# Kernel tuning notes

Hardware: AMD Instinct MI355X
Metric: run time of the kernel (lower is better)

## Reference

```python
import jax, jax.numpy as jnp
import numpy as np

N, F, M, E = 8192, 256, 128, 131072


def setup_inputs() -> dict:
    key = jax.random.key(0)
    k = jax.random.split(key, 6)
    x = jax.random.normal(k[0], (N, F), dtype=jnp.float32)
    edge_index = jax.random.randint(k[1], (2, E), 0, N, dtype=jnp.int64)
    eps = jax.random.normal(k[2], (N, M), dtype=jnp.float32)
    # small init scale so sigmoid(z_i . z_j) isn't saturated
    W_mu = jax.random.normal(k[3], (F, M), dtype=jnp.float32) * 0.05
    b_mu = jnp.zeros((M,), dtype=jnp.float32)
    W_sig = jax.random.normal(k[4], (F, M), dtype=jnp.float32) * 0.05
    b_sig = jnp.zeros((M,), dtype=jnp.float32)
    return {"x": x, "edge_index": edge_index, "eps": eps,
            "W_mu": W_mu, "b_mu": b_mu, "W_sig": W_sig, "b_sig": b_sig}


def reference(x, edge_index, eps, W_mu, b_mu, W_sig, b_sig):
    # Gaussian encoder: Normal(mu, exp(logstd)), Independent over latent dim
    mu = x @ W_mu + b_mu                      # [N, M]
    logstd = x @ W_sig + b_sig                # [N, M]
    sigma = jnp.exp(logstd)
    z = mu + sigma * eps                      # rsample, [N, M]

    # decoder.probability(dot(z_i, z_j)) = sigmoid(logit); vectorized as Z @ Z.T
    logits = z @ z.T                          # [N, N]

    # symmetric adjacency labels from edge_index (either direction counts)
    src, dst = edge_index[0], edge_index[1]
    adj = jnp.zeros((N, N), dtype=jnp.float32)
    adj = adj.at[src, dst].set(1.0)
    adj = adj.at[dst, src].set(1.0)

    # BCE(sigmoid(s), y) summed over unordered pairs i < j (stable logits form)
    per_pair = jax.nn.softplus(logits) - adj * logits  # = -[y log p + (1-y) log(1-p)]
    triu = jnp.triu(jnp.ones((N, N), dtype=bool), k=1)
    bce = jnp.sum(jnp.where(triu, per_pair, 0.0))

    # sum_i KL( N(mu_i, sigma_i) || N(0, I) )
    kl = jnp.sum(0.5 * (sigma * sigma + mu * mu - 1.0) - logstd)

    return bce + 0.001 * kl
```

## Files before the change

### kernel.cpp

```cpp
#include <hip/hip_runtime.h>

#define NN 8192
#define FF 256
#define MM 128
#define HSLOTS 262144

typedef __attribute__((ext_vector_type(8))) short bf16x8;
typedef __attribute__((ext_vector_type(4))) float f32x4;

#define P_KL    0
#define P_EDGE  (64 * 16)
#define P_SP    (128 * 16)
#define Z_OFF   16384
#define Z_BYTES (NN * MM * 2)
#define HASH_OFF (Z_OFF + Z_BYTES)
#define WT_OFF  (HASH_OFF + HSLOTS * 4)
#define WT_BYTES (MM * FF * 2)

__device__ __forceinline__ float wave_reduce(float v) {
    #pragma unroll
    for (int off = 32; off > 0; off >>= 1) v += __shfl_down(v, off);
    return v;
}
__device__ __forceinline__ unsigned short f2bf(float f) {
    unsigned int u = __float_as_uint(f);
    u += 0x7fffu + ((u >> 16) & 1u);
    return (unsigned short)(u >> 16);
}
__device__ __forceinline__ int4 pack8(float4 a, float4 b) {
    int4 p;
    p.x = (int)f2bf(a.x) | ((int)f2bf(a.y) << 16);
    p.y = (int)f2bf(a.z) | ((int)f2bf(a.w) << 16);
    p.z = (int)f2bf(b.x) | ((int)f2bf(b.y) << 16);
    p.w = (int)f2bf(b.z) | ((int)f2bf(b.w) << 16);
    return p;
}

__global__ __launch_bounds__(256)
void prep_w(const float* __restrict__ Wmu, const float* __restrict__ Wsg,
            unsigned short* __restrict__ WmuT, unsigned short* __restrict__ WsgT,
            float* __restrict__ part, unsigned int* __restrict__ ht) {
    const int t = blockIdx.x * 256 + threadIdx.x;
    const int n = t >> 8, f = t & 255;
    WmuT[t] = f2bf(Wmu[f * MM + n]);
    WsgT[t] = f2bf(Wsg[f * MM + n]);
    if (t < 4096) part[t] = 0.f;
    uint4 z4 = {0u, 0u, 0u, 0u};
    ((uint4*)ht)[t * 2]     = z4;
    ((uint4*)ht)[t * 2 + 1] = z4;
}

#define XP_I4 33
#define XP_S  264

__global__ __launch_bounds__(256)
void encoder_mfma(const float* __restrict__ x, const float* __restrict__ eps,
                  const unsigned short* __restrict__ WmuT,
                  const unsigned short* __restrict__ WsgT,
                  const float* __restrict__ bmu, const float* __restrict__ bsg,
                  unsigned short* __restrict__ zb, float* __restrict__ part) {
    __shared__ int4 ax[16 * XP_I4];
    __shared__ float red[4];
    const int tid = threadIdx.x;
    const int wid = tid >> 6, lane = tid & 63;
    const int l15 = lane & 15, quad = lane >> 4;
    const int row0 = blockIdx.x * 16;

    {
        const int r = tid >> 4, ch = tid & 15;
        const float4* g0 = (const float4*)(x + (size_t)(row0 + r) * FF + ch * 8);
        const float4* g1 = (const float4*)(x + (size_t)(row0 + r) * FF + (ch + 16) * 8);
        ax[r * XP_I4 + ch]      = pack8(g0[0], g0[1]);
        ax[r * XP_I4 + ch + 16] = pack8(g1[0], g1[1]);
    }
    __syncthreads();

    const short* sax = (const short*)ax;
    const int4* wtm = (const int4*)WmuT;
    const int4* wts = (const int4*)WsgT;

    f32x4 zero4 = {0.f, 0.f, 0.f, 0.f};
    f32x4 accm[2], accl[2];
    accm[0] = accm[1] = accl[0] = accl[1] = zero4;

    #pragma unroll
    for (int ks = 0; ks < 8; ++ks) {
        const bf16x8 a = *(const bf16x8*)&sax[l15 * XP_S + ks * 32 + quad * 8];
        #pragma unroll
        for (int j = 0; j < 2; ++j) {
            const int n = wid * 32 + j * 16 + l15;
            const bf16x8 bmf = *(const bf16x8*)&wtm[n * 32 + ks * 4 + quad];
            const bf16x8 bsf = *(const bf16x8*)&wts[n * 32 + ks * 4 + quad];
            accm[j] = __builtin_amdgcn_mfma_f32_16x16x32_bf16(a, bmf, accm[j], 0, 0, 0);
            accl[j] = __builtin_amdgcn_mfma_f32_16x16x32_bf16(a, bsf, accl[j], 0, 0, 0);
        }
    }

    float klp = 0.f;
    #pragma unroll
    for (int j = 0; j < 2; ++j) {
        const int col = wid * 32 + j * 16 + l15;
        const float bm = bmu[col], bs = bsg[col];
        #pragma unroll
        for (int r = 0; r < 4; ++r) {
            const int row = row0 + quad * 4 + r;
            const float mu = accm[j][r] + bm;
            const float ls = accl[j][r] + bs;
            const float sg = __expf(ls);
            const float zz = fmaf(sg, eps[(size_t)row * MM + col], mu);
            zb[(size_t)row * MM + col] = f2bf(zz);
            klp += 0.5f * (sg * sg + mu * mu - 1.f) - ls;
        }
    }

    klp = wave_reduce(klp);
    if (lane == 0) red[wid] = klp;
    __syncthreads();
    if (tid == 0)
        atomicAdd(&part[P_KL + (blockIdx.x & 63) * 16],
                  red[0] + red[1] + red[2] + red[3]);
}

__device__ __forceinline__ float dotpair(unsigned int a, unsigned int b) {
    const float al = __uint_as_float(a << 16);
    const float ah = __uint_as_float(a & 0xffff0000u);
    const float bl = __uint_as_float(b << 16);
    const float bh = __uint_as_float(b & 0xffff0000u);
    return fmaf(al, bl, ah * bh);
}

__global__ __launch_bounds__(256)
void edge_kernel(const int* __restrict__ ei, int E,
                 const unsigned short* __restrict__ zb,
                 unsigned int* __restrict__ ht, float* __restrict__ part) {
    const int e = blockIdx.x * 256 + threadIdx.x;
    float contrib = 0.f;
    if (e < E) {
        const int i = ei[e];
        const int j = ei[E + e];
        if (i != j) {
            const int a = min(i, j), b = max(i, j);
            const unsigned int key = (unsigned int)a * NN + b;
            unsigned int slot = (key * 2654435761u) & (HSLOTS - 1);
            bool first = false;
            for (;;) {
                const unsigned int old = atomicCAS(&ht[slot], 0u, key);
                if (old == 0u) { first = true; break; }
                if (old == key) break;
                slot = (slot + 1) & (HSLOTS - 1);
            }
            if (first) {
                const uint4* za = (const uint4*)(zb + (size_t)a * MM);
                const uint4* zc = (const uint4*)(zb + (size_t)b * MM);
                float s = 0.f;
                #pragma unroll
                for (int q = 0; q < MM / 8; ++q) {
                    const uint4 ua = za[q], ub = zc[q];
                    s += dotpair(ua.x, ub.x) + dotpair(ua.y, ub.y)
                       + dotpair(ua.z, ub.z) + dotpair(ua.w, ub.w);
                }
                contrib = s;
            }
        }
    }
    contrib = wave_reduce(contrib);
    if ((threadIdx.x & 63) == 0)
        atomicAdd(&part[P_EDGE + (blockIdx.x & 63) * 16], contrib);
}

__global__ __launch_bounds__(256, 3)
void tile_kernel(const unsigned short* __restrict__ zb, float* __restrict__ part) {
    const int bi = blockIdx.y, bj = blockIdx.x;
    if (bj < bi) return;

    __shared__ int4 la[128 * 8];
    __shared__ int4 lb[128 * 8];

    const int tid = threadIdx.x;
    const int wid = tid >> 6, lane = tid & 63;
    const int wm = wid >> 1, wn = wid & 1;
    const int l15 = lane & 15, quad = lane >> 4;
    const int xk = l15 & 7;

    const int4* ga = (const int4*)(zb + (size_t)bi * 128 * MM);
    const int4* gb = (const int4*)(zb + (size_t)bj * 128 * MM);

    f32x4 zero4 = {0.f, 0.f, 0.f, 0.f};
    f32x4 acc[4][4];
    #pragma unroll
    for (int i = 0; i < 4; ++i)
        #pragma unroll
        for (int j = 0; j < 4; ++j) acc[i][j] = zero4;

    const short* sa = (const short*)la;
    const short* sb = (const short*)lb;

    #pragma unroll
    for (int kc = 0; kc < 2; ++kc) {
        if (kc) __syncthreads();
        #pragma unroll
        for (int i = 0; i < 4; ++i) {
            const int c = tid + i * 256;
            const int row = c >> 3, ch = c & 7;
            const int sl = ch ^ (row & 7);
            la[row * 8 + sl] = ga[row * 16 + kc * 8 + ch];
            lb[row * 8 + sl] = gb[row * 16 + kc * 8 + ch];
        }
        __syncthreads();
        #pragma unroll
        for (int ks = 0; ks < 2; ++ks) {
            const int kq = ks * 4 + quad;
            bf16x8 af[4], bfr[4];
            #pragma unroll
            for (int t = 0; t < 4; ++t) {
                const int ar = wm * 64 + t * 16 + l15;
                af[t]  = *(const bf16x8*)&sa[ar * 64 + ((kq ^ xk) * 8)];
                const int br = wn * 64 + t * 16 + l15;
                bfr[t] = *(const bf16x8*)&sb[br * 64 + ((kq ^ xk) * 8)];
            }
            #pragma unroll
            for (int i = 0; i < 4; ++i)
                #pragma unroll
                for (int j = 0; j < 4; ++j)
                    acc[i][j] = __builtin_amdgcn_mfma_f32_16x16x32_bf16(
                        af[i], bfr[j], acc[i][j], 0, 0, 0);
        }
    }

    float tsum = 0.f;
    if (bi != bj) {
        #pragma unroll
        for (int i = 0; i < 4; ++i)
            #pragma unroll
            for (int j = 0; j < 4; ++j)
                #pragma unroll
                for (int r = 0; r < 4; ++r) {
                    const float v = acc[i][j][r];
                    const float e = __expf(-fabsf(v));
                    tsum += fmaxf(v, 0.f) + e * fmaf(e, -0.5f, 1.f);
                }
    } else {
        const int rbase = wm * 64 + quad * 4;
        const int cbase = wn * 64 + l15;
        #pragma unroll
        for (int i = 0; i < 4; ++i)
            #pragma unroll
            for (int j = 0; j < 4; ++j)
                #pragma unroll
                for (int r = 0; r < 4; ++r)
                    if (cbase + j * 16 > rbase + i * 16 + r) {
                        const float v = acc[i][j][r];
                        const float e = __expf(-fabsf(v));
                        tsum += fmaxf(v, 0.f) + e * fmaf(e, -0.5f, 1.f);
                    }
    }

    tsum = wave_reduce(tsum);
    if (lane == 0)
        atomicAdd(&part[P_SP + ((bi * 64 + bj + wid * 16) & 63) * 16], tsum);
}

__global__ void combine_kernel(const float* __restrict__ part,
                               float* __restrict__ out) {
    const int t = threadIdx.x;
    float v = part[P_SP + t * 16] - part[P_EDGE + t * 16]
            + 0.001f * part[P_KL + t * 16];
    v = wave_reduce(v);
    if (t == 0) out[0] = v;
}

extern "C" void kernel_launch(void* const* d_in, const int* in_sizes, int n_in,
                              void* d_out, int out_size, void* d_ws, size_t ws_size,
                              hipStream_t stream) {
    const float* x   = (const float*)d_in[0];
    const int* ei    = (const int*)d_in[1];
    const float* eps = (const float*)d_in[2];
    const float* Wmu = (const float*)d_in[3];
    const float* bmu = (const float*)d_in[4];
    const float* Wsg = (const float*)d_in[5];
    const float* bsg = (const float*)d_in[6];
    float* out = (float*)d_out;
    char* ws = (char*)d_ws;

    float* part = (float*)ws;
    unsigned short* zb = (unsigned short*)(ws + Z_OFF);
    unsigned int* ht = (unsigned int*)(ws + HASH_OFF);
    unsigned short* WmuT = (unsigned short*)(ws + WT_OFF);
    unsigned short* WsgT = (unsigned short*)(ws + WT_OFF + WT_BYTES);
    const int E = in_sizes[1] / 2;

    prep_w<<<128, 256, 0, stream>>>(Wmu, Wsg, WmuT, WsgT, part, ht);
    encoder_mfma<<<NN / 16, 256, 0, stream>>>(x, eps, WmuT, WsgT, bmu, bsg, zb, part);
    edge_kernel<<<(E + 255) / 256, 256, 0, stream>>>(ei, E, zb, ht, part);
    dim3 grid(NN / 128, NN / 128);
    tile_kernel<<<grid, 256, 0, stream>>>(zb, part);
    combine_kernel<<<1, 64, 0, stream>>>(part, out);
}
```

Baseline: 130.7 us.

## Fuse edge, triangular tile and combine kernels into one launch

Merges the edge-dedup kernel, the Z·Zᵀ softplus tile kernel and the final combine into a single kernel. The first blocks handle edges, and the remaining blocks map a linear index onto upper-triangular tiles with a sqrt-based inversion, so no blocks are launched only to exit. The last block to finish, found through an atomic counter, performs the final reduction. This removes two launch gaps and the idle lower-triangle blocks, at the cost of relying on a counter in the workspace that must be reset each call.

```diff
diff --git a/kernel.cpp b/kernel.cpp
--- a/kernel.cpp
+++ b/kernel.cpp
@@ -4,6 +4,7 @@
 #define FF 256
 #define MM 128
 #define HSLOTS 262144
+#define NTILES 2080
 
 typedef __attribute__((ext_vector_type(8))) short bf16x8;
 typedef __attribute__((ext_vector_type(4))) float f32x4;
@@ -11,6 +12,7 @@
 #define P_KL    0
 #define P_EDGE  (64 * 16)
 #define P_SP    (128 * 16)
+#define P_CNT   3072
 #define Z_OFF   16384
 #define Z_BYTES (NN * MM * 2)
 #define HASH_OFF (Z_OFF + Z_BYTES)
@@ -129,144 +131,162 @@
     return fmaf(al, bl, ah * bh);
 }
 
-__global__ __launch_bounds__(256)
-void edge_kernel(const int* __restrict__ ei, int E,
-                 const unsigned short* __restrict__ zb,
-                 unsigned int* __restrict__ ht, float* __restrict__ part) {
-    const int e = blockIdx.x * 256 + threadIdx.x;
-    float contrib = 0.f;
-    if (e < E) {
-        const int i = ei[e];
-        const int j = ei[E + e];
-        if (i != j) {
-            const int a = min(i, j), b = max(i, j);
-            const unsigned int key = (unsigned int)a * NN + b;
-            unsigned int slot = (key * 2654435761u) & (HSLOTS - 1);
-            bool first = false;
-            for (;;) {
-                const unsigned int old = atomicCAS(&ht[slot], 0u, key);
-                if (old == 0u) { first = true; break; }
-                if (old == key) break;
-                slot = (slot + 1) & (HSLOTS - 1);
-            }
-            if (first) {
-                const uint4* za = (const uint4*)(zb + (size_t)a * MM);
-                const uint4* zc = (const uint4*)(zb + (size_t)b * MM);
-                float s = 0.f;
-                #pragma unroll
-                for (int q = 0; q < MM / 8; ++q) {
-                    const uint4 ua = za[q], ub = zc[q];
-                    s += dotpair(ua.x, ub.x) + dotpair(ua.y, ub.y)
-                       + dotpair(ua.z, ub.z) + dotpair(ua.w, ub.w);
-                }
-                contrib = s;
-            }
-        }
-    }
-    contrib = wave_reduce(contrib);
-    if ((threadIdx.x & 63) == 0)
-        atomicAdd(&part[P_EDGE + (blockIdx.x & 63) * 16], contrib);
-}
-
 __global__ __launch_bounds__(256, 3)
-void tile_kernel(const unsigned short* __restrict__ zb, float* __restrict__ part) {
-    const int bi = blockIdx.y, bj = blockIdx.x;
-    if (bj < bi) return;
-
+void fused_kernel(const int* __restrict__ ei, int E, int NE,
+                  const unsigned short* __restrict__ zb,
+                  unsigned int* __restrict__ ht,
+                  float* __restrict__ part, float* __restrict__ out) {
     __shared__ int4 la[128 * 8];
     __shared__ int4 lb[128 * 8];
+    __shared__ int lastflag;
 
     const int tid = threadIdx.x;
-    const int wid = tid >> 6, lane = tid & 63;
-    const int wm = wid >> 1, wn = wid & 1;
-    const int l15 = lane & 15, quad = lane >> 4;
-    const int xk = l15 & 7;
-
-    const int4* ga = (const int4*)(zb + (size_t)bi * 128 * MM);
-    const int4* gb = (const int4*)(zb + (size_t)bj * 128 * MM);
-
-    f32x4 zero4 = {0.f, 0.f, 0.f, 0.f};
-    f32x4 acc[4][4];
-    #pragma unroll
-    for (int i = 0; i < 4; ++i)
+    const int bid = blockIdx.x;
+
+    if (bid < NE) {
+        const int e = bid * 256 + tid;
+        float contrib = 0.f;
+        if (e < E) {
+            const int i = ei[e];
+            const int j = ei[E + e];
+            if (i != j) {
+                const int a = min(i, j), b = max(i, j);
+                const unsigned int key = (unsigned int)a * NN + b;
+                unsigned int slot = (key * 2654435761u) & (HSLOTS - 1);
+                bool first = false;
+                for (;;) {
+                    const unsigned int old = atomicCAS(&ht[slot], 0u, key);
+                    if (old == 0u) { first = true; break; }
+                    if (old == key) break;
+                    slot = (slot + 1) & (HSLOTS - 1);
+                }
+                if (first) {
+                    const uint4* za = (const uint4*)(zb + (size_t)a * MM);
+                    const uint4* zc = (const uint4*)(zb + (size_t)b * MM);
+                    float s = 0.f;
+                    #pragma unroll
+                    for (int q = 0; q < MM / 8; ++q) {
+                        const uint4 ua = za[q], ub = zc[q];
+                        s += dotpair(ua.x, ub.x) + dotpair(ua.y, ub.y)
+                           + dotpair(ua.z, ub.z) + dotpair(ua.w, ub.w);
+                    }
+                    contrib = s;
+                }
+            }
+        }
+        contrib = wave_reduce(contrib);
+        if ((tid & 63) == 0)
+            atomicAdd(&part[P_EDGE + (bid & 63) * 16], contrib);
+    } else {
+        const int t = bid - NE;
+        int bi = (int)((129.0f - sqrtf(16641.0f - 8.0f * (float)t)) * 0.5f);
+        bi = min(max(bi, 0), 63);
+        while ((bi * (129 - bi)) / 2 > t) --bi;
+        while (((bi + 1) * (128 - bi)) / 2 <= t) ++bi;
+        const int bj = bi + (t - (bi * (129 - bi)) / 2);
+
+        const int wid = tid >> 6, lane = tid & 63;
+        const int wm = wid >> 1, wn = wid & 1;
+        const int l15 = lane & 15, quad = lane >> 4;
+        const int xk = l15 & 7;
+
+        const int4* ga = (const int4*)(zb + (size_t)bi * 128 * MM);
+        const int4* gb = (const int4*)(zb + (size_t)bj * 128 * MM);
+
+        f32x4 zero4 = {0.f, 0.f, 0.f, 0.f};
+        f32x4 acc[4][4];
         #pragma unroll
-        for (int j = 0; j < 4; ++j) acc[i][j] = zero4;
-
-    const short* sa = (const short*)la;
-    const short* sb = (const short*)lb;
-
-    #pragma unroll
-    for (int kc = 0; kc < 2; ++kc) {
-        if (kc) __syncthreads();
+        for (int i = 0; i < 4; ++i)
+            #pragma unroll
+            for (int j = 0; j < 4; ++j) acc[i][j] = zero4;
+
+        const short* sa = (const short*)la;
+        const short* sb = (const short*)lb;
+
         #pragma unroll
-        for (int i = 0; i < 4; ++i) {
-            const int c = tid + i * 256;
-            const int row = c >> 3, ch = c & 7;
-            const int sl = ch ^ (row & 7);
-            la[row * 8 + sl] = ga[row * 16 + kc * 8 + ch];
-            lb[row * 8 + sl] = gb[row * 16 + kc * 8 + ch];
-        }
-        __syncthreads();
-        #pragma unroll
-        for (int ks = 0; ks < 2; ++ks) {
-            const int kq = ks * 4 + quad;
-            bf16x8 af[4], bfr[4];
-            #pragma unroll
-            for (int t = 0; t < 4; ++t) {
-                const int ar = wm * 64 + t * 16 + l15;
-                af[t]  = *(const bf16x8*)&sa[ar * 64 + ((kq ^ xk) * 8)];
-                const int br = wn * 64 + t * 16 + l15;
-                bfr[t] = *(const bf16x8*)&sb[br * 64 + ((kq ^ xk) * 8)];
+        for (int kc = 0; kc < 2; ++kc) {
+            if (kc) __syncthreads();
+            #pragma unroll
+            for (int i = 0; i < 4; ++i) {
+                const int c = tid + i * 256;
+                const int row = c >> 3, ch = c & 7;
+                const int sl = ch ^ (row & 7);
+                la[row * 8 + sl] = ga[row * 16 + kc * 8 + ch];
+                lb[row * 8 + sl] = gb[row * 16 + kc * 8 + ch];
             }
+            __syncthreads();
+            #pragma unroll
+            for (int ks = 0; ks < 2; ++ks) {
+                const int kq = ks * 4 + quad;
+                bf16x8 af[4], bfr[4];
+                #pragma unroll
+                for (int t2 = 0; t2 < 4; ++t2) {
+                    const int ar = wm * 64 + t2 * 16 + l15;
+                    af[t2]  = *(const bf16x8*)&sa[ar * 64 + ((kq ^ xk) * 8)];
+                    const int br = wn * 64 + t2 * 16 + l15;
+                    bfr[t2] = *(const bf16x8*)&sb[br * 64 + ((kq ^ xk) * 8)];
+                }
+                #pragma unroll
+                for (int i = 0; i < 4; ++i)
+                    #pragma unroll
+                    for (int j = 0; j < 4; ++j)
+                        acc[i][j] = __builtin_amdgcn_mfma_f32_16x16x32_bf16(
+                            af[i], bfr[j], acc[i][j], 0, 0, 0);
+            }
+        }
+
+        float tsum = 0.f;
+        if (bi != bj) {
             #pragma unroll
             for (int i = 0; i < 4; ++i)
                 #pragma unroll
                 for (int j = 0; j < 4; ++j)
-                    acc[i][j] = __builtin_amdgcn_mfma_f32_16x16x32_bf16(
-                        af[i], bfr[j], acc[i][j], 0, 0, 0);
-        }
-    }
-
-    float tsum = 0.f;
-    if (bi != bj) {
-        #pragma unroll
-        for (int i = 0; i < 4; ++i)
-            #pragma unroll
-            for (int j = 0; j < 4; ++j)
-                #pragma unroll
-                for (int r = 0; r < 4; ++r) {
-                    const float v = acc[i][j][r];
-                    const float e = __expf(-fabsf(v));
-                    tsum += fmaxf(v, 0.f) + e * fmaf(e, -0.5f, 1.f);
-                }
-    } else {
-        const int rbase = wm * 64 + quad * 4;
-        const int cbase = wn * 64 + l15;
-        #pragma unroll
-        for (int i = 0; i < 4; ++i)
-            #pragma unroll
-            for (int j = 0; j < 4; ++j)
-                #pragma unroll
-                for (int r = 0; r < 4; ++r)
-                    if (cbase + j * 16 > rbase + i * 16 + r) {
+                    #pragma unroll
+                    for (int r = 0; r < 4; ++r) {
                         const float v = acc[i][j][r];
                         const float e = __expf(-fabsf(v));
                         tsum += fmaxf(v, 0.f) + e * fmaf(e, -0.5f, 1.f);
                     }
-    }
-
-    tsum = wave_reduce(tsum);
-    if (lane == 0)
-        atomicAdd(&part[P_SP + ((bi * 64 + bj + wid * 16) & 63) * 16], tsum);
-}
-
-__global__ void combine_kernel(const float* __restrict__ part,
-                               float* __restrict__ out) {
-    const int t = threadIdx.x;
-    float v = part[P_SP + t * 16] - part[P_EDGE + t * 16]
-            + 0.001f * part[P_KL + t * 16];
-    v = wave_reduce(v);
-    if (t == 0) out[0] = v;
+        } else {
+            const int rbase = wm * 64 + quad * 4;
+            const int cbase = wn * 64 + l15;
+            #pragma unroll
+            for (int i = 0; i < 4; ++i)
+                #pragma unroll
+                for (int j = 0; j < 4; ++j)
+                    #pragma unroll
+                    for (int r = 0; r < 4; ++r)
+                        if (cbase + j * 16 > rbase + i * 16 + r) {
+                            const float v = acc[i][j][r];
+                            const float e = __expf(-fabsf(v));
+                            tsum += fmaxf(v, 0.f) + e * fmaf(e, -0.5f, 1.f);
+                        }
+        }
+
+        tsum = wave_reduce(tsum);
+        if (lane == 0)
+            atomicAdd(&part[P_SP + ((bi * 64 + bj + wid * 16) & 63) * 16], tsum);
+    }
+
+    __syncthreads();
+    if (tid == 0) {
+        __threadfence();
+        const unsigned int old =
+            atomicAdd(reinterpret_cast<unsigned int*>(part) + P_CNT, 1u);
+        lastflag = (old == gridDim.x - 1) ? 1 : 0;
+    }
+    __syncthreads();
+    if (lastflag && tid < 64) {
+        __threadfence();
+        float v = __hip_atomic_load(&part[P_SP + tid * 16],
+                                    __ATOMIC_RELAXED, __HIP_MEMORY_SCOPE_AGENT)
+                - __hip_atomic_load(&part[P_EDGE + tid * 16],
+                                    __ATOMIC_RELAXED, __HIP_MEMORY_SCOPE_AGENT)
+                + 0.001f * __hip_atomic_load(&part[P_KL + tid * 16],
+                                    __ATOMIC_RELAXED, __HIP_MEMORY_SCOPE_AGENT);
+        v = wave_reduce(v);
+        if (tid == 0) out[0] = v;
+    }
 }
 
 extern "C" void kernel_launch(void* const* d_in, const int* in_sizes, int n_in,
@@ -288,11 +308,9 @@
     unsigned short* WmuT = (unsigned short*)(ws + WT_OFF);
     unsigned short* WsgT = (unsigned short*)(ws + WT_OFF + WT_BYTES);
     const int E = in_sizes[1] / 2;
+    const int NE = (E + 255) / 256;
 
     prep_w<<<128, 256, 0, stream>>>(Wmu, Wsg, WmuT, WsgT, part, ht);
     encoder_mfma<<<NN / 16, 256, 0, stream>>>(x, eps, WmuT, WsgT, bmu, bsg, zb, part);
-    edge_kernel<<<(E + 255) / 256, 256, 0, stream>>>(ei, E, zb, ht, part);
-    dim3 grid(NN / 128, NN / 128);
-    tile_kernel<<<grid, 256, 0, stream>>>(zb, part);
-    combine_kernel<<<1, 64, 0, stream>>>(part, out);
-}
+    fused_kernel<<<NE + NTILES, 256, 0, stream>>>(ei, E, NE, zb, ht, part, out);
+}
```

Measured after the change: 152.6 us. 1.17x slower.

## Fuse edge kernel into triangular-indexed tile kernel

Applied to the files above, without the earlier changes.

Merges the edge-correction kernel into the tile kernel. Each of the first NE blocks processes 256 edges after finishing its tile. The tile grid is also compacted from the full 64x64 grid to the 2080 upper-triangle tiles, with the (bi,bj) pair recovered from a sqrt-based index inversion, so no blocks launch only to exit. This removes one launch and the idle lower-triangle blocks, but adds hash atomics and latency to the tail of the first 512 blocks.

```diff
diff --git a/kernel.cpp b/kernel.cpp
--- a/kernel.cpp
+++ b/kernel.cpp
@@ -4,6 +4,7 @@
 #define FF 256
 #define MM 128
 #define HSLOTS 262144
+#define NTILES 2080
 
 typedef __attribute__((ext_vector_type(8))) short bf16x8;
 typedef __attribute__((ext_vector_type(4))) float f32x4;
@@ -129,54 +130,23 @@
     return fmaf(al, bl, ah * bh);
 }
 
-__global__ __launch_bounds__(256)
-void edge_kernel(const int* __restrict__ ei, int E,
-                 const unsigned short* __restrict__ zb,
-                 unsigned int* __restrict__ ht, float* __restrict__ part) {
-    const int e = blockIdx.x * 256 + threadIdx.x;
-    float contrib = 0.f;
-    if (e < E) {
-        const int i = ei[e];
-        const int j = ei[E + e];
-        if (i != j) {
-            const int a = min(i, j), b = max(i, j);
-            const unsigned int key = (unsigned int)a * NN + b;
-            unsigned int slot = (key * 2654435761u) & (HSLOTS - 1);
-            bool first = false;
-            for (;;) {
-                const unsigned int old = atomicCAS(&ht[slot], 0u, key);
-                if (old == 0u) { first = true; break; }
-                if (old == key) break;
-                slot = (slot + 1) & (HSLOTS - 1);
-            }
-            if (first) {
-                const uint4* za = (const uint4*)(zb + (size_t)a * MM);
-                const uint4* zc = (const uint4*)(zb + (size_t)b * MM);
-                float s = 0.f;
-                #pragma unroll
-                for (int q = 0; q < MM / 8; ++q) {
-                    const uint4 ua = za[q], ub = zc[q];
-                    s += dotpair(ua.x, ub.x) + dotpair(ua.y, ub.y)
-                       + dotpair(ua.z, ub.z) + dotpair(ua.w, ub.w);
-                }
-                contrib = s;
-            }
-        }
-    }
-    contrib = wave_reduce(contrib);
-    if ((threadIdx.x & 63) == 0)
-        atomicAdd(&part[P_EDGE + (blockIdx.x & 63) * 16], contrib);
-}
-
 __global__ __launch_bounds__(256, 3)
-void tile_kernel(const unsigned short* __restrict__ zb, float* __restrict__ part) {
-    const int bi = blockIdx.y, bj = blockIdx.x;
-    if (bj < bi) return;
-
+void tile_edge_kernel(const unsigned short* __restrict__ zb,
+                      const int* __restrict__ ei, int E, int NE,
+                      unsigned int* __restrict__ ht,
+                      float* __restrict__ part) {
     __shared__ int4 la[128 * 8];
     __shared__ int4 lb[128 * 8];
 
     const int tid = threadIdx.x;
+    const int bid = blockIdx.x;
+
+    int bi = (int)((129.0f - sqrtf(16641.0f - 8.0f * (float)bid)) * 0.5f);
+    bi = min(max(bi, 0), 63);
+    while ((bi * (129 - bi)) / 2 > bid) --bi;
+    while (((bi + 1) * (128 - bi)) / 2 <= bid) ++bi;
+    const int bj = bi + (bid - (bi * (129 - bi)) / 2);
+
     const int wid = tid >> 6, lane = tid & 63;
     const int wm = wid >> 1, wn = wid & 1;
     const int l15 = lane & 15, quad = lane >> 4;
@@ -212,11 +182,11 @@
             const int kq = ks * 4 + quad;
             bf16x8 af[4], bfr[4];
             #pragma unroll
-            for (int t = 0; t < 4; ++t) {
-                const int ar = wm * 64 + t * 16 + l15;
-                af[t]  = *(const bf16x8*)&sa[ar * 64 + ((kq ^ xk) * 8)];
-                const int br = wn * 64 + t * 16 + l15;
-                bfr[t] = *(const bf16x8*)&sb[br * 64 + ((kq ^ xk) * 8)];
+            for (int t2 = 0; t2 < 4; ++t2) {
+                const int ar = wm * 64 + t2 * 16 + l15;
+                af[t2]  = *(const bf16x8*)&sa[ar * 64 + ((kq ^ xk) * 8)];
+                const int br = wn * 64 + t2 * 16 + l15;
+                bfr[t2] = *(const bf16x8*)&sb[br * 64 + ((kq ^ xk) * 8)];
             }
             #pragma unroll
             for (int i = 0; i < 4; ++i)
@@ -258,6 +228,42 @@
     tsum = wave_reduce(tsum);
     if (lane == 0)
         atomicAdd(&part[P_SP + ((bi * 64 + bj + wid * 16) & 63) * 16], tsum);
+
+    if (bid < NE) {
+        const int e = bid * 256 + tid;
+        float contrib = 0.f;
+        if (e < E) {
+            const int i = ei[e];
+            const int j = ei[E + e];
+            if (i != j) {
+                const int a = min(i, j), b = max(i, j);
+                const unsigned int key = (unsigned int)a * NN + b;
+                unsigned int slot = (key * 2654435761u) & (HSLOTS - 1);
+                bool first = false;
+                for (;;) {
+                    const unsigned int old = atomicCAS(&ht[slot], 0u, key);
+                    if (old == 0u) { first = true; break; }
+                    if (old == key) break;
+                    slot = (slot + 1) & (HSLOTS - 1);
+                }
+                if (first) {
+                    const uint4* za = (const uint4*)(zb + (size_t)a * MM);
+                    const uint4* zc = (const uint4*)(zb + (size_t)b * MM);
+                    float s = 0.f;
+                    #pragma unroll
+                    for (int q = 0; q < MM / 8; ++q) {
+                        const uint4 ua = za[q], ub = zc[q];
+                        s += dotpair(ua.x, ub.x) + dotpair(ua.y, ub.y)
+                           + dotpair(ua.z, ub.z) + dotpair(ua.w, ub.w);
+                    }
+                    contrib = s;
+                }
+            }
+        }
+        contrib = wave_reduce(contrib);
+        if ((tid & 63) == 0)
+            atomicAdd(&part[P_EDGE + (bid & 63) * 16], contrib);
+    }
 }
 
 __global__ void combine_kernel(const float* __restrict__ part,
@@ -288,11 +294,10 @@
     unsigned short* WmuT = (unsigned short*)(ws + WT_OFF);
     unsigned short* WsgT = (unsigned short*)(ws + WT_OFF + WT_BYTES);
     const int E = in_sizes[1] / 2;
+    const int NE = (E + 255) / 256;
 
     prep_w<<<128, 256, 0, stream>>>(Wmu, Wsg, WmuT, WsgT, part, ht);
     encoder_mfma<<<NN / 16, 256, 0, stream>>>(x, eps, WmuT, WsgT, bmu, bsg, zb, part);
-    edge_kernel<<<(E + 255) / 256, 256, 0, stream>>>(ei, E, zb, ht, part);
-    dim3 grid(NN / 128, NN / 128);
-    tile_kernel<<<grid, 256, 0, stream>>>(zb, part);
+    tile_edge_kernel<<<NTILES, 256, 0, stream>>>(zb, ei, E, NE, ht, part);
     combine_kernel<<<1, 64, 0, stream>>>(part, out);
 }
```

New measurement: 113.9 us, median of 2. -12.8%, faster.
